# Performance work log

Hardware: AMD Instinct MI355X
Metric: run time of the kernel (lower is better)

Reference implementation:

```python
import jax, jax.numpy as jnp
import numpy as np

B, T, I, H = 512, 1024, 64, 256


def setup_inputs() -> dict:
    key = jax.random.key(0)
    ks = jax.random.split(key, 12)
    s_ih = 1.0 / np.sqrt(H)
    inp = {
        "x": jax.random.normal(ks[0], (B, T, I), dtype=jnp.float32),
        # LSTMCell params (PyTorch layout): W_ih (4H, I), W_hh (4H, H), gate order i,f,g,o
        "W_ih": jax.random.uniform(ks[1], (4 * H, I), minval=-s_ih, maxval=s_ih),
        "W_hh": jax.random.uniform(ks[2], (4 * H, H), minval=-s_ih, maxval=s_ih),
        "b_ih": jax.random.uniform(ks[3], (4 * H,), minval=-s_ih, maxval=s_ih),
        "b_hh": jax.random.uniform(ks[4], (4 * H,), minval=-s_ih, maxval=s_ih),
        # heads
        "W_dir": jax.random.uniform(ks[5], (1, H), minval=-s_ih, maxval=s_ih),
        "b_dir": jnp.zeros((1,), jnp.float32),
        "W_q": jax.random.uniform(ks[6], (5, H), minval=-s_ih, maxval=s_ih),
        "b_q": jnp.zeros((5,), jnp.float32),
        "W_rr": jax.random.uniform(ks[7], (1, H), minval=-s_ih, maxval=s_ih),
        "b_rr": jnp.zeros((1,), jnp.float32),
        "W_sl": jax.random.uniform(ks[8], (1, H), minval=-s_ih, maxval=s_ih),
        "b_sl": jnp.zeros((1,), jnp.float32),
    }
    return inp


def _lstm_last_hidden(x, W_ih, W_hh, b_ih, b_hh):
    # Precompute input projection for all timesteps in one GEMM: (B,T,4H)
    xg = jnp.einsum("bti,gi->btg", x, W_ih) + b_ih + b_hh
    xg = jnp.transpose(xg, (1, 0, 2))  # (T,B,4H)
    h0 = jnp.zeros((x.shape[0], W_hh.shape[1]), x.dtype)
    c0 = jnp.zeros_like(h0)

    def step(carry, xg_t):
        h, c = carry
        gates = xg_t + h @ W_hh.T  # (B,4H)
        i, f, g, o = jnp.split(gates, 4, axis=-1)
        i = jax.nn.sigmoid(i)
        f = jax.nn.sigmoid(f)
        g = jnp.tanh(g)
        o = jax.nn.sigmoid(o)
        c = f * c + i * g
        h = o * jnp.tanh(c)
        return (h, c), None

    (h, _), _ = jax.lax.scan(step, (h0, c0), xg)
    return h


def reference(x, W_ih, W_hh, b_ih, b_hh, W_dir, b_dir, W_q, b_q, W_rr, b_rr, W_sl, b_sl):
    h = _lstm_last_hidden(x, W_ih, W_hh, b_ih, b_hh)  # (B,H)
    direction = jnp.tanh(h @ W_dir.T + b_dir)          # (B,1)
    quality = h @ W_q.T + b_q                          # (B,5)
    reward = h @ W_rr.T + b_rr                         # (B,1)
    sl_prob = jax.nn.sigmoid(h @ W_sl.T + b_sl)        # (B,1)
    return jnp.concatenate([direction, quality, reward, sl_prob], axis=1)
```

## Files before the change

kernel.cpp:

```cpp
#include <hip/hip_runtime.h>


typedef __attribute__((ext_vector_type(4))) float f32x4;
typedef __attribute__((ext_vector_type(4))) unsigned int u32x4;
typedef __attribute__((ext_vector_type(8))) short bf16x8;
typedef __attribute__((ext_vector_type(8))) unsigned short u16x8;

#define T_SZ 1024
#define I_SZ 64
#define H_SZ 256
#define KFRAGS 10
#define MROWS 16
#define NTHREADS 512
#define NBLK 256

#define HB_PAR 65536
#define HB_GRP 2048
#define HB_FRG 256

#define FLAG_STRIDE 16
#define NFLAG (32 * 8 * FLAG_STRIDE)

#define WT_FRAGS (64 * KFRAGS * 64)
#define WS_BIAS_OFF  (WT_FRAGS * 16)
#define WS_HBUF_OFF  (WS_BIAS_OFF + 4096)
#define WS_FLAGS_OFF (WS_HBUF_OFF + 2 * HB_PAR * 4)
#define SPIN_CAP (1 << 20)

__device__ __forceinline__ unsigned short f2bf(float f) {
    unsigned int u = __builtin_bit_cast(unsigned int, f);
    unsigned int r = (u + 0x7FFFu + ((u >> 16) & 1u)) >> 16;
    return (unsigned short)r;
}
__device__ __forceinline__ float bf2f(unsigned short s) {
    unsigned int u = ((unsigned int)s) << 16;
    return __builtin_bit_cast(float, u);
}
__device__ __forceinline__ float sigm(float x) {
    return 1.0f / (1.0f + exp2f(-1.44269504f * x));
}
__device__ __forceinline__ float tanhfast(float x) {
    float e = exp2f(2.88539008f * x);
    return 1.0f - 2.0f / (e + 1.0f);
}

__global__ void prep_kernel(const float* __restrict__ W_ih,
                            const float* __restrict__ W_hh,
                            const float* __restrict__ b_ih,
                            const float* __restrict__ b_hh,
                            unsigned short* __restrict__ Wt,
                            float* __restrict__ bias,
                            unsigned int* __restrict__ hbuf,
                            int* __restrict__ flags) {
    int gid = blockIdx.x * blockDim.x + threadIdx.x;
    if (gid < WT_FRAGS) {
        int lane = gid & 63;
        int rest = gid >> 6;
        int kf = rest % KFRAGS;
        int gt = rest / KFRAGS;
        int ns = gt >> 3, w = gt & 7;
        int n = lane & 15;
        int g = (n & 3) * 256 + ns * 32 + w * 4 + (n >> 2);
        int k0 = kf * 32 + (lane >> 4) * 8;
        u16x8 v;
        #pragma unroll
        for (int j = 0; j < 8; ++j) {
            int k = k0 + j;
            float wv = (k < H_SZ) ? W_hh[g * H_SZ + k]
                                  : W_ih[g * I_SZ + (k - H_SZ)];
            v[j] = f2bf(wv);
        }
        ((u16x8*)Wt)[gid] = v;
    } else if (gid < WT_FRAGS + 1024) {
        int j = gid - WT_FRAGS;
        bias[j] = b_ih[j] + b_hh[j];
    } else if (gid < WT_FRAGS + 1024 + 2 * HB_PAR) {
        hbuf[gid - WT_FRAGS - 1024] = 0u;
    } else if (gid < WT_FRAGS + 1024 + 2 * HB_PAR + NFLAG) {
        flags[gid - WT_FRAGS - 1024 - 2 * HB_PAR] = 0;
    }
}

__global__ __launch_bounds__(NTHREADS)
void lstm_kernel(const float* __restrict__ x,
                 const unsigned short* __restrict__ Wt,
                 const float* __restrict__ bias,
                 unsigned int* __restrict__ hbuf,
                 int* __restrict__ flags,
                 const float* __restrict__ W_dir, const float* __restrict__ b_dir,
                 const float* __restrict__ W_q,   const float* __restrict__ b_q,
                 const float* __restrict__ W_rr,  const float* __restrict__ b_rr,
                 const float* __restrict__ W_sl,  const float* __restrict__ b_sl,
                 float* __restrict__ out)
{
    __shared__ float tr[8 * 16 * 17];
    __shared__ unsigned int hstage[MROWS * 128];

    const int tid  = threadIdx.x;
    const int lane = tid & 63;
    const int wave = tid >> 6;
    const int ns   = blockIdx.x >> 5;
    const int bg   = blockIdx.x & 31;
    const int b0   = bg * MROWS;

    bf16x8 wf[KFRAGS];
    #pragma unroll
    for (int kf = 0; kf < KFRAGS; ++kf)
        wf[kf] = *(const bf16x8*)(Wt +
            ((size_t)((ns * 8 + wave) * KFRAGS + kf) * 64 + lane) * 8);

    const int er = lane & 15;
    const int hc = lane >> 4;
    const int jg = ns * 32 + wave * 4 + hc;
    const float bi0 = bias[jg];
    const float bi1 = bias[256 + jg];
    const float bi2 = bias[512 + jg];
    const float bi3 = bias[768 + jg];

    float* trw = &tr[wave * (16 * 17)];
    const int n_idx = lane & 15;
    const int rb = (lane >> 4) * 4;

    const float* xbase = x + (size_t)(b0 + er) * (T_SZ * I_SZ) + hc * 8;
    int* myflag = flags + (bg * 8 + ns) * FLAG_STRIDE;
    const int* fpoll = flags + (bg * 8 + (lane & 7)) * FLAG_STRIDE;

    const int cp = wave * 2 + ((lane >> 5) & 1);
    unsigned int* const hw_base = hbuf + (size_t)bg * HB_GRP + ns * HB_FRG
                                  + (er + 16 * (cp >> 2)) * 4 + (cp & 3);
    const unsigned int* const hr_base = hbuf + (size_t)bg * HB_GRP + lane * 4;

    float creg = 0.0f;

    f32x4 xa = *(const f32x4*)xbase;
    f32x4 xb = *(const f32x4*)(xbase + 4);
    f32x4 xc = *(const f32x4*)(xbase + 32);
    f32x4 xd = *(const f32x4*)(xbase + 36);
    u32x4 xf0u, xf1u;
    {
        unsigned p0, p1, p2, p3, p4, p5, p6, p7;
        asm("v_cvt_pk_bf16_f32 %0, %1, %2" : "=v"(p0) : "v"(xa[0]), "v"(xa[1]));
        asm("v_cvt_pk_bf16_f32 %0, %1, %2" : "=v"(p1) : "v"(xa[2]), "v"(xa[3]));
        asm("v_cvt_pk_bf16_f32 %0, %1, %2" : "=v"(p2) : "v"(xb[0]), "v"(xb[1]));
        asm("v_cvt_pk_bf16_f32 %0, %1, %2" : "=v"(p3) : "v"(xb[2]), "v"(xb[3]));
        asm("v_cvt_pk_bf16_f32 %0, %1, %2" : "=v"(p4) : "v"(xc[0]), "v"(xc[1]));
        asm("v_cvt_pk_bf16_f32 %0, %1, %2" : "=v"(p5) : "v"(xc[2]), "v"(xc[3]));
        asm("v_cvt_pk_bf16_f32 %0, %1, %2" : "=v"(p6) : "v"(xd[0]), "v"(xd[1]));
        asm("v_cvt_pk_bf16_f32 %0, %1, %2" : "=v"(p7) : "v"(xd[2]), "v"(xd[3]));
        xf0u = (u32x4){p0, p1, p2, p3};
        xf1u = (u32x4){p4, p5, p6, p7};
    }

    for (int t = 0; t < T_SZ; ++t) {
        const size_t rpar = (size_t)(t & 1) * HB_PAR;
        const size_t wpar = (size_t)((t + 1) & 1) * HB_PAR;

        if (t) {
            int spin = 0;
            while (true) {
                int v;
                asm volatile("global_load_dword %0, %1, off sc0 sc1\n\t"
                             "s_waitcnt vmcnt(0)"
                             : "=v"(v) : "v"(fpoll) : "memory");
                if (__all(v >= t)) break;
                if (++spin > SPIN_CAP) break;
            }
            __builtin_amdgcn_sched_barrier(0);
        }

        u32x4 hv0, hv1, hv2, hv3, hv4, hv5, hv6, hv7;
        {
            const unsigned int* hp = hr_base + rpar;
            asm volatile("global_load_dwordx4 %0, %1, off sc0 sc1" : "=v"(hv0) : "v"(hp) : "memory");
            asm volatile("global_load_dwordx4 %0, %1, off sc0 sc1" : "=v"(hv1) : "v"(hp + HB_FRG) : "memory");
            asm volatile("global_load_dwordx4 %0, %1, off sc0 sc1" : "=v"(hv2) : "v"(hp + 2 * HB_FRG) : "memory");
            asm volatile("global_load_dwordx4 %0, %1, off sc0 sc1" : "=v"(hv3) : "v"(hp + 3 * HB_FRG) : "memory");
            asm volatile("global_load_dwordx4 %0, %1, off sc0 sc1" : "=v"(hv4) : "v"(hp + 4 * HB_FRG) : "memory");
            asm volatile("global_load_dwordx4 %0, %1, off sc0 sc1" : "=v"(hv5) : "v"(hp + 5 * HB_FRG) : "memory");
            asm volatile("global_load_dwordx4 %0, %1, off sc0 sc1" : "=v"(hv6) : "v"(hp + 6 * HB_FRG) : "memory");
            asm volatile("global_load_dwordx4 %0, %1, off sc0 sc1" : "=v"(hv7) : "v"(hp + 7 * HB_FRG) : "memory");
        }
        f32x4 accA = {0.0f, 0.0f, 0.0f, 0.0f};
        f32x4 accB = {0.0f, 0.0f, 0.0f, 0.0f};
        accA = __builtin_amdgcn_mfma_f32_16x16x32_bf16(__builtin_bit_cast(bf16x8, xf0u), wf[8], accA, 0, 0, 0);
        accB = __builtin_amdgcn_mfma_f32_16x16x32_bf16(__builtin_bit_cast(bf16x8, xf1u), wf[9], accB, 0, 0, 0);
        asm volatile("s_waitcnt vmcnt(0)" ::: "memory");
        __builtin_amdgcn_sched_barrier(0);

        accA = __builtin_amdgcn_mfma_f32_16x16x32_bf16(__builtin_bit_cast(bf16x8, hv0), wf[0], accA, 0, 0, 0);
        accB = __builtin_amdgcn_mfma_f32_16x16x32_bf16(__builtin_bit_cast(bf16x8, hv1), wf[1], accB, 0, 0, 0);
        accA = __builtin_amdgcn_mfma_f32_16x16x32_bf16(__builtin_bit_cast(bf16x8, hv2), wf[2], accA, 0, 0, 0);
        accB = __builtin_amdgcn_mfma_f32_16x16x32_bf16(__builtin_bit_cast(bf16x8, hv3), wf[3], accB, 0, 0, 0);
        accA = __builtin_amdgcn_mfma_f32_16x16x32_bf16(__builtin_bit_cast(bf16x8, hv4), wf[4], accA, 0, 0, 0);
        accB = __builtin_amdgcn_mfma_f32_16x16x32_bf16(__builtin_bit_cast(bf16x8, hv5), wf[5], accB, 0, 0, 0);
        accA = __builtin_amdgcn_mfma_f32_16x16x32_bf16(__builtin_bit_cast(bf16x8, hv6), wf[6], accA, 0, 0, 0);
        accB = __builtin_amdgcn_mfma_f32_16x16x32_bf16(__builtin_bit_cast(bf16x8, hv7), wf[7], accB, 0, 0, 0);
        f32x4 acc = accA + accB;

        #pragma unroll
        for (int q = 0; q < 4; ++q)
            trw[(rb + q) * 17 + n_idx] = acc[q];
        float gi = trw[er * 17 + hc * 4 + 0] + bi0;
        float gf = trw[er * 17 + hc * 4 + 1] + bi1;
        float gg = trw[er * 17 + hc * 4 + 2] + bi2;
        float go = trw[er * 17 + hc * 4 + 3] + bi3;

        float ii = sigm(gi), ff = sigm(gf), gG = tanhfast(gg), oo = sigm(go);
        float c = ff * creg + ii * gG;
        creg = c;
        float h = oo * tanhfast(c);

        unsigned hu = (unsigned)f2bf(h);
        unsigned pj = (unsigned)__shfl_xor((int)hu, 16);
        if (!(lane & 16)) {
            unsigned v = hu | (pj << 16);
            unsigned int* sp = hw_base + wpar;
            asm volatile("global_store_dword %0, %1, off sc0 sc1" :: "v"(sp), "v"(v) : "memory");
        }

        {
            const float* xp = xbase + (size_t)((t + 1 < T_SZ) ? t + 1 : t) * I_SZ;
            asm volatile("global_load_dwordx4 %0, %1, off" : "=v"(xa) : "v"(xp) : "memory");
            asm volatile("global_load_dwordx4 %0, %1, off" : "=v"(xb) : "v"(xp + 4) : "memory");
            asm volatile("global_load_dwordx4 %0, %1, off" : "=v"(xc) : "v"(xp + 32) : "memory");
            asm volatile("global_load_dwordx4 %0, %1, off" : "=v"(xd) : "v"(xp + 36) : "memory");
        }
        asm volatile("s_waitcnt vmcnt(4)" ::: "memory");
        __builtin_amdgcn_s_barrier();
        if (tid == 0) {
            int fv = t + 1;
            asm volatile("global_store_dword %0, %1, off sc0 sc1" :: "v"(myflag), "v"(fv) : "memory");
        }
        asm volatile("s_waitcnt vmcnt(0)" ::: "memory");
        __builtin_amdgcn_sched_barrier(0);
        {
            unsigned p0, p1, p2, p3, p4, p5, p6, p7;
            asm("v_cvt_pk_bf16_f32 %0, %1, %2" : "=v"(p0) : "v"(xa[0]), "v"(xa[1]));
            asm("v_cvt_pk_bf16_f32 %0, %1, %2" : "=v"(p1) : "v"(xa[2]), "v"(xa[3]));
            asm("v_cvt_pk_bf16_f32 %0, %1, %2" : "=v"(p2) : "v"(xb[0]), "v"(xb[1]));
            asm("v_cvt_pk_bf16_f32 %0, %1, %2" : "=v"(p3) : "v"(xb[2]), "v"(xb[3]));
            asm("v_cvt_pk_bf16_f32 %0, %1, %2" : "=v"(p4) : "v"(xc[0]), "v"(xc[1]));
            asm("v_cvt_pk_bf16_f32 %0, %1, %2" : "=v"(p5) : "v"(xc[2]), "v"(xc[3]));
            asm("v_cvt_pk_bf16_f32 %0, %1, %2" : "=v"(p6) : "v"(xd[0]), "v"(xd[1]));
            asm("v_cvt_pk_bf16_f32 %0, %1, %2" : "=v"(p7) : "v"(xd[2]), "v"(xd[3]));
            xf0u = (u32x4){p0, p1, p2, p3};
            xf1u = (u32x4){p4, p5, p6, p7};
        }
    }

    if (ns == 0) {
        {
            int spin = 0;
            while (true) {
                int v;
                asm volatile("global_load_dword %0, %1, off sc0 sc1\n\t"
                             "s_waitcnt vmcnt(0)"
                             : "=v"(v) : "v"(fpoll) : "memory");
                if (__all(v >= T_SZ)) break;
                if (++spin > SPIN_CAP) break;
            }
            __builtin_amdgcn_sched_barrier(0);
        }
        {
            int kf = tid >> 6, l = tid & 63;
            const unsigned int* hp = hbuf + (size_t)bg * HB_GRP
                                     + kf * HB_FRG + l * 4;
            u32x4 hv;
            asm volatile("global_load_dwordx4 %0, %1, off sc0 sc1" : "=v"(hv) : "v"(hp) : "memory");
            asm volatile("s_waitcnt vmcnt(0)" ::: "memory");
            __builtin_amdgcn_sched_barrier(0);
            int row = l & 15;
            int cw = kf * 16 + (l >> 4) * 4;
            hstage[row * 128 + cw + 0] = hv[0];
            hstage[row * 128 + cw + 1] = hv[1];
            hstage[row * 128 + cw + 2] = hv[2];
            hstage[row * 128 + cw + 3] = hv[3];
        }
        __syncthreads();
        if (tid < MROWS * 8) {
            int r = tid >> 3, cc = tid & 7;
            const float* wrow;
            float bb;
            if (cc == 0)      { wrow = W_dir;                 bb = b_dir[0]; }
            else if (cc <= 5) { wrow = W_q + (cc - 1) * H_SZ; bb = b_q[cc - 1]; }
            else if (cc == 6) { wrow = W_rr;                  bb = b_rr[0]; }
            else              { wrow = W_sl;                  bb = b_sl[0]; }
            float s = bb;
            for (int k = 0; k < H_SZ; ++k) {
                unsigned u = hstage[r * 128 + (k >> 1)];
                unsigned short hs = (k & 1) ? (unsigned short)(u >> 16)
                                            : (unsigned short)(u & 0xFFFF);
                s += bf2f(hs) * wrow[k];
            }
            float v = (cc == 0) ? tanhfast(s) : (cc == 7) ? sigm(s) : s;
            out[(b0 + r) * 8 + cc] = v;
        }
    }
}

extern "C" void kernel_launch(void* const* d_in, const int* in_sizes, int n_in,
                              void* d_out, int out_size, void* d_ws, size_t ws_size,
                              hipStream_t stream) {
    const float* x     = (const float*)d_in[0];
    const float* W_ih  = (const float*)d_in[1];
    const float* W_hh  = (const float*)d_in[2];
    const float* b_ih  = (const float*)d_in[3];
    const float* b_hh  = (const float*)d_in[4];
    const float* W_dir = (const float*)d_in[5];
    const float* b_dir = (const float*)d_in[6];
    const float* W_q   = (const float*)d_in[7];
    const float* b_q   = (const float*)d_in[8];
    const float* W_rr  = (const float*)d_in[9];
    const float* b_rr  = (const float*)d_in[10];
    const float* W_sl  = (const float*)d_in[11];
    const float* b_sl  = (const float*)d_in[12];

    unsigned short* Wt = (unsigned short*)d_ws;
    float* bias        = (float*)((char*)d_ws + WS_BIAS_OFF);
    unsigned int* hbuf = (unsigned int*)((char*)d_ws + WS_HBUF_OFF);
    int* flags         = (int*)((char*)d_ws + WS_FLAGS_OFF);
    float* outp        = (float*)d_out;

    prep_kernel<<<692, 256, 0, stream>>>(W_ih, W_hh, b_ih, b_hh, Wt, bias,
                                         hbuf, flags);

    void* args[] = {(void*)&x, (void*)&Wt, (void*)&bias, (void*)&hbuf,
                    (void*)&flags, (void*)&W_dir, (void*)&b_dir, (void*)&W_q,
                    (void*)&b_q, (void*)&W_rr, (void*)&b_rr, (void*)&W_sl,
                    (void*)&b_sl, (void*)&outp};
    hipLaunchCooperativeKernel((void*)lstm_kernel, dim3(NBLK), dim3(NTHREADS),
                               args, 0, stream);
}
```

Baseline: 3.176 ms.

## Halve block count by giving each wave two gate tiles

Each wave now computes two 16-column gate tiles instead of one, so the kernel launches 128 blocks instead of 256 and the per-step flag synchronization is across 4 blocks per batch group instead of 8. The goal is to cut cross-block polling and synchronization cost in the per-timestep barrier, and to reuse loaded h fragments across two MFMA chains. In exchange it doubles register use for weights and the per-wave serial work per step, and uses fewer CUs. Flag stride is also widened to 64.

```diff
diff --git a/kernel.cpp b/kernel.cpp
--- a/kernel.cpp
+++ b/kernel.cpp
@@ -12,14 +12,14 @@
 #define KFRAGS 10
 #define MROWS 16
 #define NTHREADS 512
-#define NBLK 256
+#define NBLK 128
 
 #define HB_PAR 65536
 #define HB_GRP 2048
 #define HB_FRG 256
 
-#define FLAG_STRIDE 16
-#define NFLAG (32 * 8 * FLAG_STRIDE)
+#define FLAG_STRIDE 64
+#define NFLAG (32 * 4 * FLAG_STRIDE)
 
 #define WT_FRAGS (64 * KFRAGS * 64)
 #define WS_BIAS_OFF  (WT_FRAGS * 16)
@@ -57,10 +57,12 @@
         int lane = gid & 63;
         int rest = gid >> 6;
         int kf = rest % KFRAGS;
-        int gt = rest / KFRAGS;
-        int ns = gt >> 3, w = gt & 7;
+        int tileid = rest / KFRAGS;
+        int t  = tileid & 1;
+        int w  = (tileid >> 1) & 7;
+        int ns = tileid >> 4;
         int n = lane & 15;
-        int g = (n & 3) * 256 + ns * 32 + w * 4 + (n >> 2);
+        int g = (n & 3) * 256 + ns * 64 + w * 8 + t * 4 + (n >> 2);
         int k0 = kf * 32 + (lane >> 4) * 8;
         u16x8 v;
         #pragma unroll
@@ -93,7 +95,7 @@
                  const float* __restrict__ W_sl,  const float* __restrict__ b_sl,
                  float* __restrict__ out)
 {
-    __shared__ float tr[8 * 16 * 17];
+    __shared__ float tr[16 * 16 * 17];
     __shared__ unsigned int hstage[MROWS * 128];
 
     const int tid  = threadIdx.x;
@@ -103,34 +105,42 @@
     const int bg   = blockIdx.x & 31;
     const int b0   = bg * MROWS;
 
-    bf16x8 wf[KFRAGS];
+    bf16x8 wf0[KFRAGS], wf1[KFRAGS];
     #pragma unroll
-    for (int kf = 0; kf < KFRAGS; ++kf)
-        wf[kf] = *(const bf16x8*)(Wt +
-            ((size_t)((ns * 8 + wave) * KFRAGS + kf) * 64 + lane) * 8);
+    for (int kf = 0; kf < KFRAGS; ++kf) {
+        wf0[kf] = *(const bf16x8*)(Wt +
+            ((size_t)((((ns * 8 + wave) * 2 + 0) * KFRAGS) + kf) * 64 + lane) * 8);
+        wf1[kf] = *(const bf16x8*)(Wt +
+            ((size_t)((((ns * 8 + wave) * 2 + 1) * KFRAGS) + kf) * 64 + lane) * 8);
+    }
 
     const int er = lane & 15;
     const int hc = lane >> 4;
-    const int jg = ns * 32 + wave * 4 + hc;
-    const float bi0 = bias[jg];
-    const float bi1 = bias[256 + jg];
-    const float bi2 = bias[512 + jg];
-    const float bi3 = bias[768 + jg];
-
-    float* trw = &tr[wave * (16 * 17)];
+    const int jg0 = ns * 64 + wave * 8 + 0 * 4 + hc;
+    const int jg1 = ns * 64 + wave * 8 + 1 * 4 + hc;
+    const float b00 = bias[jg0],       b01 = bias[256 + jg0];
+    const float b02 = bias[512 + jg0], b03 = bias[768 + jg0];
+    const float b10 = bias[jg1],       b11 = bias[256 + jg1];
+    const float b12 = bias[512 + jg1], b13 = bias[768 + jg1];
+
+    float* trw0 = &tr[(wave * 2 + 0) * (16 * 17)];
+    float* trw1 = &tr[(wave * 2 + 1) * (16 * 17)];
     const int n_idx = lane & 15;
     const int rb = (lane >> 4) * 4;
 
     const float* xbase = x + (size_t)(b0 + er) * (T_SZ * I_SZ) + hc * 8;
-    int* myflag = flags + (bg * 8 + ns) * FLAG_STRIDE;
-    const int* fpoll = flags + (bg * 8 + (lane & 7)) * FLAG_STRIDE;
-
-    const int cp = wave * 2 + ((lane >> 5) & 1);
-    unsigned int* const hw_base = hbuf + (size_t)bg * HB_GRP + ns * HB_FRG
-                                  + (er + 16 * (cp >> 2)) * 4 + (cp & 3);
+    int* myflag = flags + (bg * 4 + ns) * FLAG_STRIDE;
+    const int* fpoll = flags + (bg * 4 + (lane & 3)) * FLAG_STRIDE;
+
+    const int P0 = ns * 32 + wave * 4 + 0 * 2 + ((lane >> 5) & 1);
+    const int P1 = ns * 32 + wave * 4 + 1 * 2 + ((lane >> 5) & 1);
+    unsigned int* const hw_base0 = hbuf + (size_t)bg * HB_GRP
+        + (P0 >> 4) * HB_FRG + (er + 16 * ((P0 >> 2) & 3)) * 4 + (P0 & 3);
+    unsigned int* const hw_base1 = hbuf + (size_t)bg * HB_GRP
+        + (P1 >> 4) * HB_FRG + (er + 16 * ((P1 >> 2) & 3)) * 4 + (P1 & 3);
     const unsigned int* const hr_base = hbuf + (size_t)bg * HB_GRP + lane * 4;
 
-    float creg = 0.0f;
+    float creg0 = 0.0f, creg1 = 0.0f;
 
     f32x4 xa = *(const f32x4*)xbase;
     f32x4 xb = *(const f32x4*)(xbase + 4);
@@ -180,42 +190,62 @@
             asm volatile("global_load_dwordx4 %0, %1, off sc0 sc1" : "=v"(hv6) : "v"(hp + 6 * HB_FRG) : "memory");
             asm volatile("global_load_dwordx4 %0, %1, off sc0 sc1" : "=v"(hv7) : "v"(hp + 7 * HB_FRG) : "memory");
         }
-        f32x4 accA = {0.0f, 0.0f, 0.0f, 0.0f};
-        f32x4 accB = {0.0f, 0.0f, 0.0f, 0.0f};
-        accA = __builtin_amdgcn_mfma_f32_16x16x32_bf16(__builtin_bit_cast(bf16x8, xf0u), wf[8], accA, 0, 0, 0);
-        accB = __builtin_amdgcn_mfma_f32_16x16x32_bf16(__builtin_bit_cast(bf16x8, xf1u), wf[9], accB, 0, 0, 0);
+        f32x4 acc0 = {0.0f, 0.0f, 0.0f, 0.0f};
+        f32x4 acc1 = {0.0f, 0.0f, 0.0f, 0.0f};
+        acc0 = __builtin_amdgcn_mfma_f32_16x16x32_bf16(__builtin_bit_cast(bf16x8, xf0u), wf0[8], acc0, 0, 0, 0);
+        acc1 = __builtin_amdgcn_mfma_f32_16x16x32_bf16(__builtin_bit_cast(bf16x8, xf0u), wf1[8], acc1, 0, 0, 0);
+        acc0 = __builtin_amdgcn_mfma_f32_16x16x32_bf16(__builtin_bit_cast(bf16x8, xf1u), wf0[9], acc0, 0, 0, 0);
+        acc1 = __builtin_amdgcn_mfma_f32_16x16x32_bf16(__builtin_bit_cast(bf16x8, xf1u), wf1[9], acc1, 0, 0, 0);
         asm volatile("s_waitcnt vmcnt(0)" ::: "memory");
         __builtin_amdgcn_sched_barrier(0);
 
-        accA = __builtin_amdgcn_mfma_f32_16x16x32_bf16(__builtin_bit_cast(bf16x8, hv0), wf[0], accA, 0, 0, 0);
-        accB = __builtin_amdgcn_mfma_f32_16x16x32_bf16(__builtin_bit_cast(bf16x8, hv1), wf[1], accB, 0, 0, 0);
-        accA = __builtin_amdgcn_mfma_f32_16x16x32_bf16(__builtin_bit_cast(bf16x8, hv2), wf[2], accA, 0, 0, 0);
-        accB = __builtin_amdgcn_mfma_f32_16x16x32_bf16(__builtin_bit_cast(bf16x8, hv3), wf[3], accB, 0, 0, 0);
-        accA = __builtin_amdgcn_mfma_f32_16x16x32_bf16(__builtin_bit_cast(bf16x8, hv4), wf[4], accA, 0, 0, 0);
-        accB = __builtin_amdgcn_mfma_f32_16x16x32_bf16(__builtin_bit_cast(bf16x8, hv5), wf[5], accB, 0, 0, 0);
-        accA = __builtin_amdgcn_mfma_f32_16x16x32_bf16(__builtin_bit_cast(bf16x8, hv6), wf[6], accA, 0, 0, 0);
-        accB = __builtin_amdgcn_mfma_f32_16x16x32_bf16(__builtin_bit_cast(bf16x8, hv7), wf[7], accB, 0, 0, 0);
-        f32x4 acc = accA + accB;
+        acc0 = __builtin_amdgcn_mfma_f32_16x16x32_bf16(__builtin_bit_cast(bf16x8, hv0), wf0[0], acc0, 0, 0, 0);
+        acc1 = __builtin_amdgcn_mfma_f32_16x16x32_bf16(__builtin_bit_cast(bf16x8, hv0), wf1[0], acc1, 0, 0, 0);
+        acc0 = __builtin_amdgcn_mfma_f32_16x16x32_bf16(__builtin_bit_cast(bf16x8, hv1), wf0[1], acc0, 0, 0, 0);
+        acc1 = __builtin_amdgcn_mfma_f32_16x16x32_bf16(__builtin_bit_cast(bf16x8, hv1), wf1[1], acc1, 0, 0, 0);
+        acc0 = __builtin_amdgcn_mfma_f32_16x16x32_bf16(__builtin_bit_cast(bf16x8, hv2), wf0[2], acc0, 0, 0, 0);
+        acc1 = __builtin_amdgcn_mfma_f32_16x16x32_bf16(__builtin_bit_cast(bf16x8, hv2), wf1[2], acc1, 0, 0, 0);
+        acc0 = __builtin_amdgcn_mfma_f32_16x16x32_bf16(__builtin_bit_cast(bf16x8, hv3), wf0[3], acc0, 0, 0, 0);
+        acc1 = __builtin_amdgcn_mfma_f32_16x16x32_bf16(__builtin_bit_cast(bf16x8, hv3), wf1[3], acc1, 0, 0, 0);
+        acc0 = __builtin_amdgcn_mfma_f32_16x16x32_bf16(__builtin_bit_cast(bf16x8, hv4), wf0[4], acc0, 0, 0, 0);
+        acc1 = __builtin_amdgcn_mfma_f32_16x16x32_bf16(__builtin_bit_cast(bf16x8, hv4), wf1[4], acc1, 0, 0, 0);
+        acc0 = __builtin_amdgcn_mfma_f32_16x16x32_bf16(__builtin_bit_cast(bf16x8, hv5), wf0[5], acc0, 0, 0, 0);
+        acc1 = __builtin_amdgcn_mfma_f32_16x16x32_bf16(__builtin_bit_cast(bf16x8, hv5), wf1[5], acc1, 0, 0, 0);
+        acc0 = __builtin_amdgcn_mfma_f32_16x16x32_bf16(__builtin_bit_cast(bf16x8, hv6), wf0[6], acc0, 0, 0, 0);
+        acc1 = __builtin_amdgcn_mfma_f32_16x16x32_bf16(__builtin_bit_cast(bf16x8, hv6), wf1[6], acc1, 0, 0, 0);
+        acc0 = __builtin_amdgcn_mfma_f32_16x16x32_bf16(__builtin_bit_cast(bf16x8, hv7), wf0[7], acc0, 0, 0, 0);
+        acc1 = __builtin_amdgcn_mfma_f32_16x16x32_bf16(__builtin_bit_cast(bf16x8, hv7), wf1[7], acc1, 0, 0, 0);
 
         #pragma unroll
-        for (int q = 0; q < 4; ++q)
-            trw[(rb + q) * 17 + n_idx] = acc[q];
-        float gi = trw[er * 17 + hc * 4 + 0] + bi0;
-        float gf = trw[er * 17 + hc * 4 + 1] + bi1;
-        float gg = trw[er * 17 + hc * 4 + 2] + bi2;
-        float go = trw[er * 17 + hc * 4 + 3] + bi3;
-
-        float ii = sigm(gi), ff = sigm(gf), gG = tanhfast(gg), oo = sigm(go);
-        float c = ff * creg + ii * gG;
-        creg = c;
-        float h = oo * tanhfast(c);
-
-        unsigned hu = (unsigned)f2bf(h);
-        unsigned pj = (unsigned)__shfl_xor((int)hu, 16);
+        for (int q = 0; q < 4; ++q) {
+            trw0[(rb + q) * 17 + n_idx] = acc0[q];
+            trw1[(rb + q) * 17 + n_idx] = acc1[q];
+        }
+        float g00 = trw0[er * 17 + hc * 4 + 0] + b00;
+        float g01 = trw0[er * 17 + hc * 4 + 1] + b01;
+        float g02 = trw0[er * 17 + hc * 4 + 2] + b02;
+        float g03 = trw0[er * 17 + hc * 4 + 3] + b03;
+        float g10 = trw1[er * 17 + hc * 4 + 0] + b10;
+        float g11 = trw1[er * 17 + hc * 4 + 1] + b11;
+        float g12 = trw1[er * 17 + hc * 4 + 2] + b12;
+        float g13 = trw1[er * 17 + hc * 4 + 3] + b13;
+
+        float i0 = sigm(g00), f0 = sigm(g01), gG0 = tanhfast(g02), o0 = sigm(g03);
+        float i1 = sigm(g10), f1 = sigm(g11), gG1 = tanhfast(g12), o1 = sigm(g13);
+        float c0 = f0 * creg0 + i0 * gG0; creg0 = c0;
+        float c1 = f1 * creg1 + i1 * gG1; creg1 = c1;
+        float h0 = o0 * tanhfast(c0);
+        float h1 = o1 * tanhfast(c1);
+
+        unsigned hu0 = (unsigned)f2bf(h0);
+        unsigned hu1 = (unsigned)f2bf(h1);
+        unsigned pj0 = (unsigned)__shfl_xor((int)hu0, 16);
+        unsigned pj1 = (unsigned)__shfl_xor((int)hu1, 16);
         if (!(lane & 16)) {
-            unsigned v = hu | (pj << 16);
-            unsigned int* sp = hw_base + wpar;
-            asm volatile("global_store_dword %0, %1, off sc0 sc1" :: "v"(sp), "v"(v) : "memory");
+            unsigned v0 = hu0 | (pj0 << 16);
+            unsigned v1 = hu1 | (pj1 << 16);
+            asm volatile("global_store_dword %0, %1, off sc0 sc1" :: "v"(hw_base0 + wpar), "v"(v0) : "memory");
+            asm volatile("global_store_dword %0, %1, off sc0 sc1" :: "v"(hw_base1 + wpar), "v"(v1) : "memory");
         }
 
         {
@@ -321,7 +351,7 @@
     int* flags         = (int*)((char*)d_ws + WS_FLAGS_OFF);
     float* outp        = (float*)d_out;
 
-    prep_kernel<<<692, 256, 0, stream>>>(W_ih, W_hh, b_ih, b_hh, Wt, bias,
+    prep_kernel<<<708, 256, 0, stream>>>(W_ih, W_hh, b_ih, b_hh, Wt, bias,
                                          hbuf, flags);
 
     void* args[] = {(void*)&x, (void*)&Wt, (void*)&bias, (void*)&hbuf,
```

Result: faster. 3.067 ms, median of 2 (-3.4%).
